# Kernel optimization log

Hardware: AMD Instinct MI355X
Metric: run time of the kernel (lower is better)

## Reference

```python
import jax, jax.numpy as jnp
import numpy as np

B, S, D = 8, 2048, 64
H = 128


def setup_inputs() -> dict:
    key = jax.random.key(0)
    k = jax.random.split(key, 5)
    X = jax.random.normal(k[0], (B, S, D), dtype=jnp.float32)
    Wi = jax.random.normal(k[1], (H, D), dtype=jnp.float32)          # init_layer weight, std=1
    bi = jax.random.normal(k[2], (H,), dtype=jnp.float32)            # init_layer bias, std=1
    Wa = jax.random.normal(k[3], (H * H, D + 1), dtype=jnp.float32) / jnp.sqrt(H)  # vf_A, std=1/sqrt(H)
    Wb = jax.random.normal(k[4], (H, D + 1), dtype=jnp.float32)      # vf_B, std=1
    return {"X": X, "Wi": Wi, "bi": bi, "Wa": Wa, "Wb": Wb}


def reference(X, Wi, bi, Wa, Wb):
    b, s, d = X.shape
    dt = 1.0 / (s - 1)
    # inp: time channel (constant dt) concatenated with scaled input -> [b, s, d+1]
    inp = jnp.concatenate([jnp.full((b, s, 1), dt, dtype=X.dtype), X * dt], axis=-1)
    y0 = X[:, 0] @ Wi.T + bi                       # [b, H]
    Bs = jnp.einsum('bsk,hk->bsh', inp[:, 1:], Wb)  # [b, s-1, H]

    def step(y, xs):
        inp_t, b_t = xs                            # [b, d+1], [b, H]
        A = (inp_t @ Wa.T).reshape(b, H, H)        # per-step transition matrix
        y_new = y + jnp.einsum('bij,bj->bi', A, y) + b_t
        return y_new, y_new

    xs = (jnp.swapaxes(inp[:, 1:], 0, 1), jnp.swapaxes(Bs, 0, 1))  # time-major
    _, ys_rest = jax.lax.scan(step, y0, xs)        # [s-1, b, H]
    ys = jnp.concatenate([y0[:, None, :], jnp.swapaxes(ys_rest, 0, 1)], axis=1)
    return ys
```

## Files before the change

### kernel.cpp

```cpp
#include <hip/hip_runtime.h>
#include <hip/hip_fp16.h>


typedef _Float16 h8 __attribute__((ext_vector_type(8)));
typedef float v4f __attribute__((ext_vector_type(4)));
typedef unsigned int uint;

constexpr int B_ = 8, S_ = 2048, D_ = 64, H_ = 128;
constexpr int T_ = S_ - 1;
constexpr int KD = D_ + 1;
constexpr float DTC = 1.0f / 2047.0f;
constexpr int L_ = 8;
constexpr int LSH = 3;
constexpr int NC = 256;

__global__ __launch_bounds__(256) void k_prep_wa(const float* __restrict__ Wa,
                                                 _Float16* __restrict__ Wa16B,
                                                 float* __restrict__ Wa0) {
  int idx = blockIdx.x * 256 + threadIdx.x;
  int r = idx >> 6, kk = idx & 63;
  int rt = r >> 4, n = r & 15;
  int kb = kk >> 5, q = (kk >> 3) & 3, jj = kk & 7;
  float v = Wa[(size_t)r * KD + 1 + kk];
  Wa16B[((((size_t)rt * 2 + kb) * 4 + q) * 16 + n) * 8 + jj] = (_Float16)v;
  if (kk == 0) Wa0[r] = Wa[(size_t)r * KD];
}

__global__ __launch_bounds__(256) void k_prep_x(const float* __restrict__ X,
                                                _Float16* __restrict__ Xs16) {
  int idx = blockIdx.x * 256 + threadIdx.x;
  int bt = idx >> 6, d = idx & 63;
  int b = bt / T_, s = bt - b * T_;
  Xs16[(size_t)bt * 64 + d] = (_Float16)(X[((size_t)b * S_ + s + 1) * D_ + d] * DTC);
}

__global__ __launch_bounds__(128) void k_y0(const float* __restrict__ X,
                                            const float* __restrict__ Wi,
                                            const float* __restrict__ bi,
                                            float* __restrict__ out,
                                            float* __restrict__ ybound) {
  int b = blockIdx.x, h = threadIdx.x;
  __shared__ float xs[D_];
  if (h < D_) xs[h] = X[(size_t)b * S_ * D_ + h];
  __syncthreads();
  float acc = bi[h];
  const float* wr = Wi + h * D_;
#pragma unroll 8
  for (int d = 0; d < D_; d++) acc += xs[d] * wr[d];
  out[(size_t)b * S_ * H_ + h] = acc;
  if (ybound) ybound[(size_t)(b * NC + 0) * H_ + h] = acc;
}

__global__ __launch_bounds__(256) void k_bs(const float* __restrict__ X,
                                            const float* __restrict__ Wb,
                                            float* __restrict__ Bs) {
  __shared__ float wb_s[H_ * KD];
  __shared__ float xs[16][D_ + 4];
  int tid = threadIdx.x;
  int bt0 = blockIdx.x * 16;
  for (int i = tid; i < H_ * KD; i += 256) wb_s[i] = Wb[i];
  for (int i = tid; i < 16 * D_; i += 256) {
    int sl = i >> 6, d = i & 63;
    int btg = bt0 + sl;
    float v = 0.f;
    if (btg < B_ * T_) {
      int b = btg / T_, s = btg - b * T_;
      v = X[((size_t)b * S_ + s + 1) * D_ + d] * DTC;
    }
    xs[sl][d] = v;
  }
  __syncthreads();
  int h = tid & 127, sh = tid >> 7;
  const float* wrow = &wb_s[h * KD];
  for (int u = 0; u < 8; u++) {
    int sl = sh * 8 + u;
    int btg = bt0 + sl;
    if (btg >= B_ * T_) break;
    float acc = wrow[0] * DTC;
#pragma unroll 8
    for (int d = 0; d < D_; d++) acc += xs[sl][d] * wrow[1 + d];
    Bs[(size_t)btg * H_ + h] = acc;
  }
}

__global__ __launch_bounds__(256) void k_amat(const _Float16* __restrict__ Xs16,
                                              const _Float16* __restrict__ Wa16B,
                                              const float* __restrict__ Wa0,
                                              _Float16* __restrict__ A_sl,
                                              int c0, int scShift) {
  __shared__ _Float16 sb[32 * 528];
  int tid = threadIdx.x;
  int w = tid >> 6, lane = tid & 63;
  int n = lane & 15, q = lane >> 4;
  int rowbase = blockIdx.x * 32;
  int SCm = ((1 << scShift) << LSH) - 1;

  h8 af[2][2];
#pragma unroll
  for (int mi = 0; mi < 2; mi++) {
    int sidx = rowbase + mi * 16 + n;
    int b = sidx >> (scShift + LSH);
    int rem = sidx & SCm;
    int cc = rem >> LSH, l = rem & (L_ - 1);
    int s = (c0 + cc) * L_ + l;
    if (s >= T_) s = T_ - 1;
    size_t btg = (size_t)b * T_ + s;
#pragma unroll
    for (int kb = 0; kb < 2; kb++)
      af[mi][kb] = *(const h8*)(Xs16 + btg * 64 + kb * 32 + q * 8);
  }

  v4f acc[2][8];
#pragma unroll
  for (int nj = 0; nj < 8; nj++) {
    int ct_g = blockIdx.y * 32 + w * 8 + nj;
    float binit = DTC * Wa0[ct_g * 16 + n];
    h8 bf0 = *(const h8*)(Wa16B + ((((size_t)ct_g * 2 + 0) * 4 + q) * 16 + n) * 8);
    h8 bf1 = *(const h8*)(Wa16B + ((((size_t)ct_g * 2 + 1) * 4 + q) * 16 + n) * 8);
#pragma unroll
    for (int mi = 0; mi < 2; mi++) {
      v4f a;
      a[0] = binit; a[1] = binit; a[2] = binit; a[3] = binit;
      a = __builtin_amdgcn_mfma_f32_16x16x32_f16(af[mi][0], bf0, a, 0, 0, 0);
      a = __builtin_amdgcn_mfma_f32_16x16x32_f16(af[mi][1], bf1, a, 0, 0, 0);
      acc[mi][nj] = a;
    }
  }
#pragma unroll
  for (int mi = 0; mi < 2; mi++)
#pragma unroll
    for (int nj = 0; nj < 8; nj++)
#pragma unroll
      for (int reg = 0; reg < 4; reg++)
        sb[(mi * 16 + q * 4 + reg) * 528 + w * 128 + ((nj * 16 + n) ^ (q * 16))] =
            (_Float16)acc[mi][nj][reg];
  __syncthreads();
#pragma unroll
  for (int it = 0; it < 8; it++) {
    int idx = tid + it * 256;
    int t = idx >> 6, u4 = idx & 63;
    int qt = (t >> 2) & 3;
    uint4 val = *(const uint4*)&sb[t * 528 + ((u4 * 8) ^ (qt * 16))];
    *(uint4*)(A_sl + (size_t)(rowbase + t) * 16384 + blockIdx.y * 512 + u4 * 8) = val;
  }
}

__global__ __launch_bounds__(256) void k_chunkmap(const _Float16* __restrict__ A_sl,
                                                  const float* __restrict__ Bs,
                                                  _Float16* __restrict__ Mr,
                                                  float* __restrict__ vch,
                                                  int c0, int scShift) {
  __shared__ _Float16 Dt[128 * 136];
  __shared__ float v32[128];
  int tid = threadIdx.x;
  int w = tid >> 6, lane = tid & 63;
  int n = lane & 15, q = lane >> 4;
  int chunk = blockIdx.x;
  int SC = 1 << scShift;
  int b = chunk >> scShift;
  int cc = chunk & (SC - 1);
  int c = c0 + cc;
  int sbase = c * L_;
  int nsteps = min(L_, T_ - sbase);
  const _Float16* Abase = A_sl + (size_t)chunk * L_ * 16384;
  size_t btb = (size_t)b * T_ + sbase;

#pragma unroll
  for (int it = 0; it < 8; it++) {
    int idx = tid + it * 256;
    int rowl = idx & 127, c8 = (idx >> 7) * 8;
    uint4 pk = *(const uint4*)(Abase + rowl * 128 + c8);
    const _Float16* hp = (const _Float16*)&pk;
#pragma unroll
    for (int cx = 0; cx < 8; cx++) Dt[(c8 + cx) * 136 + rowl] = hp[cx];
  }
  if (tid < 128) v32[tid] = Bs[btb * 128 + tid];
  h8 idE, idO;
#pragma unroll
  for (int jj = 0; jj < 8; jj++) {
    idE[jj] = (_Float16)((q * 8 + jj == n) ? 1.f : 0.f);
    idO[jj] = (_Float16)((q * 8 + jj == 16 + n) ? 1.f : 0.f);
  }
  __syncthreads();

  v4f acc[2][8];
#pragma unroll
  for (int mi = 0; mi < 2; mi++) {
    int row0 = (2 * w + mi) * 16 + q * 4;
#pragma unroll
    for (int nj = 0; nj < 8; nj++) {
      int col = nj * 16 + n;
      union { uint2 u; _Float16 h[4]; } m2;
      m2.u = *(const uint2*)&Dt[col * 136 + row0];
#pragma unroll
      for (int reg = 0; reg < 4; reg++) acc[mi][nj][reg] = (float)m2.h[reg];
    }
  }

  int r0 = 2 * w * 16 + n, r1 = r0 + 16;
  h8 afA[2][4], afB[2][4];

#define LOADA(dst, l)                                                                \
  {                                                                                  \
    const _Float16* Ag = Abase + (size_t)(l) * 16384;                                \
    _Pragma("unroll")                                                                \
    for (int mi = 0; mi < 2; mi++)                                                   \
      _Pragma("unroll")                                                              \
      for (int kb = 0; kb < 4; kb++)                                                 \
        dst[mi][kb] = *(const h8*)(Ag + ((2 * w + mi) * 16 + n) * 128 + kb * 32 + q * 8); \
  }

#define STEPQ(af, l)                                                                 \
  {                                                                                  \
    _Pragma("unroll")                                                                \
    for (int nj = 0; nj < 8; nj++) {                                                 \
      h8 bfr[4];                                                                     \
      _Pragma("unroll")                                                              \
      for (int kb = 0; kb < 4; kb++)                                                 \
        bfr[kb] = *(const h8*)&Dt[(nj * 16 + n) * 136 + kb * 32 + q * 8];            \
      _Pragma("unroll")                                                              \
      for (int mi = 0; mi < 2; mi++) {                                               \
        _Pragma("unroll")                                                            \
        for (int kb = 0; kb < 4; kb++)                                               \
          acc[mi][nj] = __builtin_amdgcn_mfma_f32_16x16x32_f16(af[mi][kb], bfr[kb], acc[mi][nj], 0, 0, 0); \
        acc[mi][nj] = __builtin_amdgcn_mfma_f32_16x16x32_f16(                        \
            af[mi][nj >> 1], (nj & 1) ? idO : idE, acc[mi][nj], 0, 0, 0);            \
      }                                                                              \
    }                                                                                \
    float dv0 = 0.f, dv1 = 0.f;                                                      \
    _Pragma("unroll")                                                                \
    for (int kb = 0; kb < 4; kb++) {                                                 \
      float4 p0 = *(const float4*)&v32[kb * 32 + q * 8];                             \
      float4 p1 = *(const float4*)&v32[kb * 32 + q * 8 + 4];                         \
      float vk[8] = {p0.x, p0.y, p0.z, p0.w, p1.x, p1.y, p1.z, p1.w};                \
      _Pragma("unroll")                                                              \
      for (int jj = 0; jj < 8; jj++) {                                               \
        dv0 += (float)af[0][kb][jj] * vk[jj];                                        \
        dv1 += (float)af[1][kb][jj] * vk[jj];                                        \
      }                                                                              \
    }                                                                                \
    dv0 += __shfl_xor(dv0, 16); dv0 += __shfl_xor(dv0, 32);                          \
    dv1 += __shfl_xor(dv1, 16); dv1 += __shfl_xor(dv1, 32);                          \
    float vold0 = v32[r0], vold1 = v32[r1];                                          \
    float bs0 = 0.f, bs1 = 0.f;                                                      \
    if (q == 0) {                                                                    \
      bs0 = Bs[(btb + (l)) * 128 + r0];                                              \
      bs1 = Bs[(btb + (l)) * 128 + r1];                                              \
    }                                                                                \
    __syncthreads();                                                                 \
    _Pragma("unroll")                                                                \
    for (int mi = 0; mi < 2; mi++) {                                                 \
      int row0 = (2 * w + mi) * 16 + q * 4;                                          \
      _Pragma("unroll")                                                              \
      for (int nj = 0; nj < 8; nj++) {                                               \
        int col = nj * 16 + n;                                                       \
        union { _Float16 h[4]; uint2 u; } pk;                                        \
        _Pragma("unroll")                                                            \
        for (int reg = 0; reg < 4; reg++) pk.h[reg] = (_Float16)acc[mi][nj][reg];    \
        *(uint2*)&Dt[col * 136 + row0] = pk.u;                                       \
      }                                                                              \
    }                                                                                \
    if (q == 0) {                                                                    \
      v32[r0] = vold0 + dv0 + bs0;                                                   \
      v32[r1] = vold1 + dv1 + bs1;                                                   \
    }                                                                                \
    __syncthreads();                                                                 \
  }

  LOADA(afA, 1);
  for (int l = 1; l < nsteps; l += 2) {
    if (l + 1 < nsteps) LOADA(afB, l + 1);
    STEPQ(afA, l);
    if (l + 2 < nsteps) LOADA(afA, l + 2);
    if (l + 1 < nsteps) STEPQ(afB, l + 1);
  }
#undef LOADA
#undef STEPQ

#pragma unroll
  for (int mi = 0; mi < 2; mi++) {
    int row0 = (2 * w + mi) * 16 + q * 4;
#pragma unroll
    for (int nj = 0; nj < 8; nj++) {
      int col = nj * 16 + n;
#pragma unroll
      for (int reg = 0; reg < 4; reg++)
        Dt[(row0 + reg) * 136 + col] = (_Float16)acc[mi][nj][reg];
    }
  }
  __syncthreads();
  _Float16* og = Mr + (size_t)chunk * 16384;
#pragma unroll
  for (int it = 0; it < 8; it++) {
    int idx = tid + it * 256;
    int rowl = idx >> 4, ch = idx & 15;
    uint4 val = *(const uint4*)&Dt[rowl * 136 + ch * 8];
    *(uint4*)(og + rowl * 128 + ch * 8) = val;
  }
  if (tid < 128) vch[(size_t)chunk * 128 + tid] = v32[tid];
}

__global__ __launch_bounds__(256) void k_comp4(const _Float16* __restrict__ in_map,
                                               const float* __restrict__ in_v,
                                               _Float16* __restrict__ out_map,
                                               float* __restrict__ out_v) {
  __shared__ _Float16 Dt[128 * 136];
  __shared__ float v32[128];
  int tid = threadIdx.x;
  int w = tid >> 6, lane = tid & 63;
  int n = lane & 15, q = lane >> 4;
  size_t nbase = (size_t)blockIdx.x * 4;

  const _Float16* P0 = in_map + nbase * 16384;
#pragma unroll
  for (int it = 0; it < 8; it++) {
    int idx = tid + it * 256;
    int rowl = idx & 127, c8 = (idx >> 7) * 8;
    uint4 pk = *(const uint4*)(P0 + rowl * 128 + c8);
    const _Float16* hp = (const _Float16*)&pk;
#pragma unroll
    for (int cx = 0; cx < 8; cx++) Dt[(c8 + cx) * 136 + rowl] = hp[cx];
  }
  if (tid < 128) v32[tid] = in_v[nbase * 128 + tid];
  h8 idE, idO;
#pragma unroll
  for (int jj = 0; jj < 8; jj++) {
    idE[jj] = (_Float16)((q * 8 + jj == n) ? 1.f : 0.f);
    idO[jj] = (_Float16)((q * 8 + jj == 16 + n) ? 1.f : 0.f);
  }
  __syncthreads();

  v4f acc[2][8];
#pragma unroll
  for (int mi = 0; mi < 2; mi++) {
    int row0 = (2 * w + mi) * 16 + q * 4;
#pragma unroll
    for (int nj = 0; nj < 8; nj++) {
      int col = nj * 16 + n;
      union { uint2 u; _Float16 h[4]; } m2;
      m2.u = *(const uint2*)&Dt[col * 136 + row0];
#pragma unroll
      for (int reg = 0; reg < 4; reg++) acc[mi][nj][reg] = (float)m2.h[reg];
    }
  }

  int r0 = 2 * w * 16 + n, r1 = r0 + 16;
  for (int j = 1; j < 4; j++) {
    const _Float16* Pj = in_map + (nbase + j) * 16384;
    h8 af[2][4];
#pragma unroll
    for (int mi = 0; mi < 2; mi++)
#pragma unroll
      for (int kb = 0; kb < 4; kb++)
        af[mi][kb] = *(const h8*)(Pj + ((2 * w + mi) * 16 + n) * 128 + kb * 32 + q * 8);
#pragma unroll
    for (int nj = 0; nj < 8; nj++) {
      h8 bfr[4];
#pragma unroll
      for (int kb = 0; kb < 4; kb++)
        bfr[kb] = *(const h8*)&Dt[(nj * 16 + n) * 136 + kb * 32 + q * 8];
#pragma unroll
      for (int mi = 0; mi < 2; mi++) {
#pragma unroll
        for (int kb = 0; kb < 4; kb++)
          acc[mi][nj] = __builtin_amdgcn_mfma_f32_16x16x32_f16(af[mi][kb], bfr[kb], acc[mi][nj], 0, 0, 0);
        acc[mi][nj] = __builtin_amdgcn_mfma_f32_16x16x32_f16(
            af[mi][nj >> 1], (nj & 1) ? idO : idE, acc[mi][nj], 0, 0, 0);
      }
    }
    float dv0 = 0.f, dv1 = 0.f;
#pragma unroll
    for (int kb = 0; kb < 4; kb++) {
      float4 p0 = *(const float4*)&v32[kb * 32 + q * 8];
      float4 p1 = *(const float4*)&v32[kb * 32 + q * 8 + 4];
      float vk[8] = {p0.x, p0.y, p0.z, p0.w, p1.x, p1.y, p1.z, p1.w};
#pragma unroll
      for (int jj = 0; jj < 8; jj++) {
        dv0 += (float)af[0][kb][jj] * vk[jj];
        dv1 += (float)af[1][kb][jj] * vk[jj];
      }
    }
    dv0 += __shfl_xor(dv0, 16); dv0 += __shfl_xor(dv0, 32);
    dv1 += __shfl_xor(dv1, 16); dv1 += __shfl_xor(dv1, 32);
    float vold0 = v32[r0], vold1 = v32[r1];
    float vj0 = 0.f, vj1 = 0.f;
    if (q == 0) {
      vj0 = in_v[(nbase + j) * 128 + r0];
      vj1 = in_v[(nbase + j) * 128 + r1];
    }
    __syncthreads();
#pragma unroll
    for (int mi = 0; mi < 2; mi++) {
      int row0 = (2 * w + mi) * 16 + q * 4;
#pragma unroll
      for (int nj = 0; nj < 8; nj++) {
        int col = nj * 16 + n;
        union { _Float16 h[4]; uint2 u; } pk;
#pragma unroll
        for (int reg = 0; reg < 4; reg++) pk.h[reg] = (_Float16)acc[mi][nj][reg];
        *(uint2*)&Dt[col * 136 + row0] = pk.u;
      }
    }
    if (q == 0) {
      v32[r0] = vold0 + dv0 + vj0;
      v32[r1] = vold1 + dv1 + vj1;
    }
    __syncthreads();
  }
#pragma unroll
  for (int mi = 0; mi < 2; mi++) {
    int row0 = (2 * w + mi) * 16 + q * 4;
#pragma unroll
    for (int nj = 0; nj < 8; nj++) {
      int col = nj * 16 + n;
#pragma unroll
      for (int reg = 0; reg < 4; reg++)
        Dt[(row0 + reg) * 136 + col] = (_Float16)acc[mi][nj][reg];
    }
  }
  __syncthreads();
  _Float16* og = out_map + (size_t)blockIdx.x * 16384;
#pragma unroll
  for (int it = 0; it < 8; it++) {
    int idx = tid + it * 256;
    int rowl = idx >> 4, ch = idx & 15;
    uint4 val = *(const uint4*)&Dt[rowl * 136 + ch * 8];
    *(uint4*)(og + rowl * 128 + ch * 8) = val;
  }
  if (tid < 128) out_v[(size_t)blockIdx.x * 128 + tid] = v32[tid];
}

__global__ __launch_bounds__(256) void k_chainsuper(const _Float16* __restrict__ Sr,
                                                    const float* __restrict__ sv,
                                                    float* __restrict__ yb,
                                                    int c0, int scShift) {
  int b = blockIdx.x, tid = threadIdx.x;
  int NS = 1 << (scShift - 2);
  int i = tid >> 1, hh = tid & 1;
  __shared__ float ybuf[128];
  __shared__ float red[128];
  if (tid < 128) ybuf[tid] = yb[(size_t)(b * NC + c0) * 128 + tid];
  __syncthreads();

  uint4 arA[8], arB[8];
  float svA, svB;

#define LOADS(ar, svv, s)                                                            \
  {                                                                                  \
    const uint4* p = (const uint4*)(Sr + (size_t)(b * NS + (s)) * 16384 + i * 128 + hh * 64); \
    _Pragma("unroll")                                                                \
    for (int u = 0; u < 8; u++) ar[u] = p[u];                                        \
    svv = sv[(size_t)(b * NS + (s)) * 128 + i];                                      \
  }

#define STEPS(ar, svv, s)                                                            \
  {                                                                                  \
    float pt = 0.f;                                                                  \
    _Pragma("unroll")                                                                \
    for (int u = 0; u < 8; u++) {                                                    \
      union { uint4 v; _Float16 h[8]; } wv; wv.v = ar[u];                            \
      _Pragma("unroll")                                                              \
      for (int k = 0; k < 8; k++) pt += (float)wv.h[k] * ybuf[hh * 64 + u * 8 + k];  \
    }                                                                                \
    if (hh) red[i] = pt;                                                             \
    __syncthreads();                                                                 \
    if (!hh) {                                                                       \
      float yn = ybuf[i] + pt + red[i] + svv;                                        \
      int cg = c0 + 4 * ((s) + 1);                                                   \
      if (cg < NC) yb[(size_t)(b * NC + cg) * 128 + i] = yn;                         \
      ybuf[i] = yn;                                                                  \
    }                                                                                \
    __syncthreads();                                                                 \
  }

  LOADS(arA, svA, 0);
  int s = 0;
  for (; s + 1 < NS; s += 2) {
    LOADS(arB, svB, s + 1);
    STEPS(arA, svA, s);
    if (s + 2 < NS) LOADS(arA, svA, s + 2);
    STEPS(arB, svB, s + 1);
  }
  if (s < NS) STEPS(arA, svA, s);
#undef LOADS
#undef STEPS
}

__global__ __launch_bounds__(256) void k_fill(const _Float16* __restrict__ Mr,
                                              const float* __restrict__ vch,
                                              float* __restrict__ yb,
                                              int c0, int scShift) {
  int tid = threadIdx.x;
  int NS = 1 << (scShift - 2);
  int b = blockIdx.x >> (scShift - 2);
  int s = blockIdx.x & (NS - 1);
  int i = tid >> 1, hh = tid & 1;
  __shared__ float ybuf[128];
  __shared__ float red[128];
  if (tid < 128) ybuf[tid] = yb[(size_t)(b * NC + c0 + 4 * s) * 128 + tid];
  __syncthreads();
  size_t node0 = ((size_t)b << scShift) + 4 * s;

  uint4 arA[8], arB[8];
  float vvA, vvB;

#define LOADF(ar, vv, k)                                                             \
  {                                                                                  \
    const uint4* p = (const uint4*)(Mr + (node0 + (k)) * 16384 + i * 128 + hh * 64); \
    _Pragma("unroll")                                                                \
    for (int u = 0; u < 8; u++) ar[u] = p[u];                                        \
    vv = vch[(node0 + (k)) * 128 + i];                                               \
  }

#define STEPF(ar, vv, k)                                                             \
  {                                                                                  \
    float pt = 0.f;                                                                  \
    _Pragma("unroll")                                                                \
    for (int u = 0; u < 8; u++) {                                                    \
      union { uint4 v; _Float16 h[8]; } wv; wv.v = ar[u];                            \
      _Pragma("unroll")                                                              \
      for (int kk = 0; kk < 8; kk++) pt += (float)wv.h[kk] * ybuf[hh * 64 + u * 8 + kk]; \
    }                                                                                \
    if (hh) red[i] = pt;                                                             \
    __syncthreads();                                                                 \
    if (!hh) {                                                                       \
      float yn = ybuf[i] + pt + red[i] + vv;                                         \
      yb[(size_t)(b * NC + c0 + 4 * s + (k) + 1) * 128 + i] = yn;                    \
      ybuf[i] = yn;                                                                  \
    }                                                                                \
    __syncthreads();                                                                 \
  }

  LOADF(arA, vvA, 0);
  LOADF(arB, vvB, 1);
  STEPF(arA, vvA, 0);
  LOADF(arA, vvA, 2);
  STEPF(arB, vvB, 1);
  STEPF(arA, vvA, 2);
#undef LOADF
#undef STEPF
}

__global__ __launch_bounds__(256) void k_emit(const _Float16* __restrict__ A_sl,
                                              const float* __restrict__ Bs,
                                              const float* __restrict__ yb,
                                              float* __restrict__ out,
                                              int c0, int scShift) {
  int tid = threadIdx.x;
  int SC = 1 << scShift;
  int b = blockIdx.x >> scShift;
  int cc = blockIdx.x & (SC - 1);
  int c = c0 + cc;
  int i = tid >> 1, hh = tid & 1;
  __shared__ float ybuf[128];
  __shared__ float red[128];
  if (tid < 128) ybuf[tid] = yb[(size_t)(b * NC + c) * 128 + tid];
  __syncthreads();
  int nst = min(L_, T_ - c * L_);
  size_t sidx0 = (size_t)blockIdx.x * L_;
  size_t btb = (size_t)b * T_ + c * L_;

  uint4 arA[8], arB[8];
  float bsA, bsB;

#define LOADR(ar, bsv, l)                                                            \
  {                                                                                  \
    const uint4* p = (const uint4*)(A_sl + (sidx0 + (l)) * 16384 + i * 128 + hh * 64); \
    _Pragma("unroll")                                                                \
    for (int u = 0; u < 8; u++) ar[u] = p[u];                                        \
    bsv = Bs[(btb + (l)) * 128 + i];                                                 \
  }

#define STEPE(ar, bsv, l)                                                            \
  {                                                                                  \
    float pt = 0.f;                                                                  \
    _Pragma("unroll")                                                                \
    for (int u = 0; u < 8; u++) {                                                    \
      union { uint4 v; _Float16 h[8]; } wv; wv.v = ar[u];                            \
      _Pragma("unroll")                                                              \
      for (int k = 0; k < 8; k++) pt += (float)wv.h[k] * ybuf[hh * 64 + u * 8 + k];  \
    }                                                                                \
    if (hh) red[i] = pt;                                                             \
    __syncthreads();                                                                 \
    if (!hh) {                                                                       \
      float yn = ybuf[i] + pt + red[i] + bsv;                                        \
      out[((size_t)b * S_ + (size_t)(c * L_ + (l) + 1)) * 128 + i] = yn;             \
      ybuf[i] = yn;                                                                  \
    }                                                                                \
    __syncthreads();                                                                 \
  }

  LOADR(arA, bsA, 0);
  for (int l = 0; l < nst; l += 2) {
    if (l + 1 < nst) LOADR(arB, bsB, l + 1);
    STEPE(arA, bsA, l);
    if (l + 2 < nst) LOADR(arA, bsA, l + 2);
    if (l + 1 < nst) STEPE(arB, bsB, l + 1);
  }
#undef LOADR
#undef STEPE
}

__global__ __launch_bounds__(256) void k_seq(const float* __restrict__ X,
                                             const float* __restrict__ Wa,
                                             const float* __restrict__ Wb,
                                             float* __restrict__ out) {
  int b = blockIdx.x, tid = threadIdx.x;
  int i = tid >> 1, hh = tid & 1;
  __shared__ float y[H_], red[H_], xs[D_], bts[H_];
  if (tid < H_) y[tid] = out[(size_t)b * S_ * H_ + tid];
  __syncthreads();
  for (int t = 1; t < S_; t++) {
    if (tid < D_) xs[tid] = X[((size_t)b * S_ + t) * D_ + tid] * DTC;
    __syncthreads();
    if (tid < H_) {
      const float* wr = Wb + tid * KD;
      float acc = wr[0] * DTC;
#pragma unroll 8
      for (int d = 0; d < D_; d++) acc += xs[d] * wr[1 + d];
      bts[tid] = acc;
    }
    float part = 0.f;
    const float* yhalf = &y[hh * 64];
    for (int j = 0; j < 64; j++) {
      const float* wr = Wa + ((size_t)(i * H_) + hh * 64 + j) * KD;
      float a = wr[0] * DTC;
#pragma unroll 8
      for (int d = 0; d < D_; d++) a += xs[d] * wr[1 + d];
      part += a * yhalf[j];
    }
    if (hh) red[i] = part;
    __syncthreads();
    if (!hh) {
      float yn = y[i] + part + red[i] + bts[i];
      out[((size_t)b * S_ + t) * H_ + i] = yn;
      y[i] = yn;
    }
    __syncthreads();
  }
}

extern "C" void kernel_launch(void* const* d_in, const int* in_sizes, int n_in,
                              void* d_out, int out_size, void* d_ws, size_t ws_size,
                              hipStream_t stream) {
  (void)in_sizes; (void)n_in; (void)out_size;
  const float* X  = (const float*)d_in[0];
  const float* Wi = (const float*)d_in[1];
  const float* bi = (const float*)d_in[2];
  const float* Wa = (const float*)d_in[3];
  const float* Wb = (const float*)d_in[4];
  float* out = (float*)d_out;
  char* ws = (char*)d_ws;

  size_t off = 0;
  auto alloc = [&](size_t bytes) { size_t o = off; off = (off + bytes + 255) & ~(size_t)255; return o; };
  size_t oBs  = alloc((size_t)B_ * T_ * 128 * 4);
  size_t oYb  = alloc((size_t)B_ * NC * 128 * 4);
  size_t oWaB = alloc((size_t)64 * 16384 * 2);
  size_t oWa0 = alloc((size_t)16384 * 4);
  size_t oXs  = alloc((size_t)B_ * T_ * 64 * 2);
  size_t fixed = off;

  const size_t APC  = (size_t)B_ * L_ * 16384 * 2;
  const size_t MRPC = (size_t)B_ * 16384 * 2;
  const size_t VCPC = (size_t)B_ * 128 * 4;
  const size_t SRPC = (size_t)B_ * 16384 * 2 / 4;
  const size_t SVPC = (size_t)B_ * 128;
  const size_t PER_SC = APC + MRPC + VCPC + SRPC + SVPC + 5 * 256;

  int SC = 0;
  if (ws_size > fixed) {
    size_t avail = ws_size - fixed;
    SC = 64;
    while (SC >= 4 && (size_t)SC * PER_SC > avail) SC >>= 1;
    if (SC < 4) SC = 0;
  }
  if (SC < 4) {
    k_y0<<<B_, 128, 0, stream>>>(X, Wi, bi, out, nullptr);
    k_seq<<<B_, 256, 0, stream>>>(X, Wa, Wb, out);
    return;
  }
  int scShift = __builtin_ctz(SC);

  size_t oMr = alloc((size_t)SC * MRPC);
  size_t oVc = alloc((size_t)SC * VCPC);
  size_t oSr = alloc((size_t)SC * SRPC);
  size_t oSv = alloc((size_t)SC * SVPC);
  size_t oA  = alloc((size_t)SC * APC);

  float*    Bs    = (float*)(ws + oBs);
  float*    yb    = (float*)(ws + oYb);
  _Float16* Wa16B = (_Float16*)(ws + oWaB);
  float*    Wa0   = (float*)(ws + oWa0);
  _Float16* Xs16  = (_Float16*)(ws + oXs);
  _Float16* Mr    = (_Float16*)(ws + oMr);
  float*    vch   = (float*)(ws + oVc);
  _Float16* Sr    = (_Float16*)(ws + oSr);
  float*    sv    = (float*)(ws + oSv);
  _Float16* A_sl  = (_Float16*)(ws + oA);

  k_prep_wa<<<4096, 256, 0, stream>>>(Wa, Wa16B, Wa0);
  k_prep_x<<<4094, 256, 0, stream>>>(X, Xs16);
  k_y0<<<B_, 128, 0, stream>>>(X, Wi, bi, out, yb);
  k_bs<<<(B_ * T_ + 15) / 16, 256, 0, stream>>>(X, Wb, Bs);

  int nslices = NC / SC;
  int chunks = B_ * SC;
  int amat_gx = (B_ * SC * L_) / 32;
  for (int si = 0; si < nslices; si++) {
    int c0 = si * SC;
    k_amat<<<dim3(amat_gx, 32), 256, 0, stream>>>(Xs16, Wa16B, Wa0, A_sl, c0, scShift);
    k_chunkmap<<<chunks, 256, 0, stream>>>(A_sl, Bs, Mr, vch, c0, scShift);
    k_comp4<<<chunks / 4, 256, 0, stream>>>(Mr, vch, Sr, sv);
    k_chainsuper<<<B_, 256, 0, stream>>>(Sr, sv, yb, c0, scShift);
    k_fill<<<chunks / 4, 256, 0, stream>>>(Mr, vch, yb, c0, scShift);
    k_emit<<<chunks, 256, 0, stream>>>(A_sl, Bs, yb, out, c0, scShift);
  }
}
```

Before: 616.1 us.

## Fuse prep kernels and fold chunk-boundary fill into emit kernel

Merges the Wa/X conversion kernels into one launch and the y0/Bs kernels into another, which cuts launch count. Removes the separate k_fill pass: each emit block now recomputes its own chunk starting state by applying up to three chunk maps from the super-chunk boundary in shared memory. This saves one launch per slice and the global round trip for boundary states. In exchange, emit blocks do redundant serial mat-vec work and read extra Mr data, and the work is uneven across blocks.

```diff
diff --git a/kernel.cpp b/kernel.cpp
--- a/kernel.cpp
+++ b/kernel.cpp
@@ -14,49 +14,55 @@
 constexpr int LSH = 3;
 constexpr int NC = 256;
 
-__global__ __launch_bounds__(256) void k_prep_wa(const float* __restrict__ Wa,
-                                                 _Float16* __restrict__ Wa16B,
-                                                 float* __restrict__ Wa0) {
-  int idx = blockIdx.x * 256 + threadIdx.x;
-  int r = idx >> 6, kk = idx & 63;
-  int rt = r >> 4, n = r & 15;
-  int kb = kk >> 5, q = (kk >> 3) & 3, jj = kk & 7;
-  float v = Wa[(size_t)r * KD + 1 + kk];
-  Wa16B[((((size_t)rt * 2 + kb) * 4 + q) * 16 + n) * 8 + jj] = (_Float16)v;
-  if (kk == 0) Wa0[r] = Wa[(size_t)r * KD];
-}
-
-__global__ __launch_bounds__(256) void k_prep_x(const float* __restrict__ X,
-                                                _Float16* __restrict__ Xs16) {
-  int idx = blockIdx.x * 256 + threadIdx.x;
-  int bt = idx >> 6, d = idx & 63;
-  int b = bt / T_, s = bt - b * T_;
-  Xs16[(size_t)bt * 64 + d] = (_Float16)(X[((size_t)b * S_ + s + 1) * D_ + d] * DTC);
-}
-
-__global__ __launch_bounds__(128) void k_y0(const float* __restrict__ X,
-                                            const float* __restrict__ Wi,
-                                            const float* __restrict__ bi,
-                                            float* __restrict__ out,
-                                            float* __restrict__ ybound) {
-  int b = blockIdx.x, h = threadIdx.x;
-  __shared__ float xs[D_];
-  if (h < D_) xs[h] = X[(size_t)b * S_ * D_ + h];
-  __syncthreads();
-  float acc = bi[h];
-  const float* wr = Wi + h * D_;
+__global__ __launch_bounds__(256) void k_prep0(const float* __restrict__ Wa,
+                                               _Float16* __restrict__ Wa16B,
+                                               float* __restrict__ Wa0,
+                                               const float* __restrict__ X,
+                                               _Float16* __restrict__ Xs16) {
+  int bx = blockIdx.x;
+  if (bx < 4096) {
+    int idx = bx * 256 + threadIdx.x;
+    int r = idx >> 6, kk = idx & 63;
+    int rt = r >> 4, n = r & 15;
+    int kb = kk >> 5, q = (kk >> 3) & 3, jj = kk & 7;
+    float v = Wa[(size_t)r * KD + 1 + kk];
+    Wa16B[((((size_t)rt * 2 + kb) * 4 + q) * 16 + n) * 8 + jj] = (_Float16)v;
+    if (kk == 0) Wa0[r] = Wa[(size_t)r * KD];
+  } else {
+    int idx = (bx - 4096) * 256 + threadIdx.x;
+    if (idx < B_ * T_ * 64) {
+      int bt = idx >> 6, d = idx & 63;
+      int b = bt / T_, s = bt - b * T_;
+      Xs16[(size_t)bt * 64 + d] = (_Float16)(X[((size_t)b * S_ + s + 1) * D_ + d] * DTC);
+    }
+  }
+}
+
+__global__ __launch_bounds__(256) void k_prep1(const float* __restrict__ X,
+                                               const float* __restrict__ Wb,
+                                               float* __restrict__ Bs,
+                                               const float* __restrict__ Wi,
+                                               const float* __restrict__ bi,
+                                               float* __restrict__ out,
+                                               float* __restrict__ yb) {
+  int tid = threadIdx.x;
+  if (blockIdx.x >= 1024) {
+    int b = blockIdx.x - 1024;
+    __shared__ float xs0[D_];
+    if (tid < D_) xs0[tid] = X[(size_t)b * S_ * D_ + tid];
+    __syncthreads();
+    if (tid < H_) {
+      float acc = bi[tid];
+      const float* wr = Wi + tid * D_;
 #pragma unroll 8
-  for (int d = 0; d < D_; d++) acc += xs[d] * wr[d];
-  out[(size_t)b * S_ * H_ + h] = acc;
-  if (ybound) ybound[(size_t)(b * NC + 0) * H_ + h] = acc;
-}
-
-__global__ __launch_bounds__(256) void k_bs(const float* __restrict__ X,
-                                            const float* __restrict__ Wb,
-                                            float* __restrict__ Bs) {
+      for (int d = 0; d < D_; d++) acc += xs0[d] * wr[d];
+      out[(size_t)b * S_ * H_ + tid] = acc;
+      yb[(size_t)(b * NC + 0) * H_ + tid] = acc;
+    }
+    return;
+  }
   __shared__ float wb_s[H_ * KD];
   __shared__ float xs[16][D_ + 4];
-  int tid = threadIdx.x;
   int bt0 = blockIdx.x * 16;
   for (int i = tid; i < H_ * KD; i += 256) wb_s[i] = Wb[i];
   for (int i = tid; i < 16 * D_; i += 256) {
@@ -486,63 +492,10 @@
 #undef STEPS
 }
 
-__global__ __launch_bounds__(256) void k_fill(const _Float16* __restrict__ Mr,
-                                              const float* __restrict__ vch,
-                                              float* __restrict__ yb,
-                                              int c0, int scShift) {
-  int tid = threadIdx.x;
-  int NS = 1 << (scShift - 2);
-  int b = blockIdx.x >> (scShift - 2);
-  int s = blockIdx.x & (NS - 1);
-  int i = tid >> 1, hh = tid & 1;
-  __shared__ float ybuf[128];
-  __shared__ float red[128];
-  if (tid < 128) ybuf[tid] = yb[(size_t)(b * NC + c0 + 4 * s) * 128 + tid];
-  __syncthreads();
-  size_t node0 = ((size_t)b << scShift) + 4 * s;
-
-  uint4 arA[8], arB[8];
-  float vvA, vvB;
-
-#define LOADF(ar, vv, k)                                                             \
-  {                                                                                  \
-    const uint4* p = (const uint4*)(Mr + (node0 + (k)) * 16384 + i * 128 + hh * 64); \
-    _Pragma("unroll")                                                                \
-    for (int u = 0; u < 8; u++) ar[u] = p[u];                                        \
-    vv = vch[(node0 + (k)) * 128 + i];                                               \
-  }
-
-#define STEPF(ar, vv, k)                                                             \
-  {                                                                                  \
-    float pt = 0.f;                                                                  \
-    _Pragma("unroll")                                                                \
-    for (int u = 0; u < 8; u++) {                                                    \
-      union { uint4 v; _Float16 h[8]; } wv; wv.v = ar[u];                            \
-      _Pragma("unroll")                                                              \
-      for (int kk = 0; kk < 8; kk++) pt += (float)wv.h[kk] * ybuf[hh * 64 + u * 8 + kk]; \
-    }                                                                                \
-    if (hh) red[i] = pt;                                                             \
-    __syncthreads();                                                                 \
-    if (!hh) {                                                                       \
-      float yn = ybuf[i] + pt + red[i] + vv;                                         \
-      yb[(size_t)(b * NC + c0 + 4 * s + (k) + 1) * 128 + i] = yn;                    \
-      ybuf[i] = yn;                                                                  \
-    }                                                                                \
-    __syncthreads();                                                                 \
-  }
-
-  LOADF(arA, vvA, 0);
-  LOADF(arB, vvB, 1);
-  STEPF(arA, vvA, 0);
-  LOADF(arA, vvA, 2);
-  STEPF(arB, vvB, 1);
-  STEPF(arA, vvA, 2);
-#undef LOADF
-#undef STEPF
-}
-
 __global__ __launch_bounds__(256) void k_emit(const _Float16* __restrict__ A_sl,
                                               const float* __restrict__ Bs,
+                                              const _Float16* __restrict__ Mr,
+                                              const float* __restrict__ vch,
                                               const float* __restrict__ yb,
                                               float* __restrict__ out,
                                               int c0, int scShift) {
@@ -554,14 +507,39 @@
   int i = tid >> 1, hh = tid & 1;
   __shared__ float ybuf[128];
   __shared__ float red[128];
-  if (tid < 128) ybuf[tid] = yb[(size_t)(b * NC + c) * 128 + tid];
-  __syncthreads();
+  int kpre = cc & 3;
+  int cbase = c - kpre;
+  if (tid < 128) ybuf[tid] = yb[(size_t)(b * NC + cbase) * 128 + tid];
+  __syncthreads();
+  size_t node0 = ((size_t)b << scShift) + (cc & ~3);
+
+  uint4 arA[8], arB[8];
+  float bsA, bsB;
+
+  for (int j = 0; j < kpre; j++) {
+    const uint4* p = (const uint4*)(Mr + (node0 + j) * 16384 + i * 128 + hh * 64);
+#pragma unroll
+    for (int u = 0; u < 8; u++) arA[u] = p[u];
+    float vv = vch[(node0 + j) * 128 + i];
+    float pt = 0.f;
+#pragma unroll
+    for (int u = 0; u < 8; u++) {
+      union { uint4 v; _Float16 h[8]; } wv; wv.v = arA[u];
+#pragma unroll
+      for (int k = 0; k < 8; k++) pt += (float)wv.h[k] * ybuf[hh * 64 + u * 8 + k];
+    }
+    if (hh) red[i] = pt;
+    __syncthreads();
+    if (!hh) {
+      float yn = ybuf[i] + pt + red[i] + vv;
+      ybuf[i] = yn;
+    }
+    __syncthreads();
+  }
+
   int nst = min(L_, T_ - c * L_);
   size_t sidx0 = (size_t)blockIdx.x * L_;
   size_t btb = (size_t)b * T_ + c * L_;
-
-  uint4 arA[8], arB[8];
-  float bsA, bsB;
 
 #define LOADR(ar, bsv, l)                                                            \
   {                                                                                  \
@@ -638,6 +616,21 @@
     }
     __syncthreads();
   }
+}
+
+__global__ __launch_bounds__(128) void k_y0f(const float* __restrict__ X,
+                                             const float* __restrict__ Wi,
+                                             const float* __restrict__ bi,
+                                             float* __restrict__ out) {
+  int b = blockIdx.x, h = threadIdx.x;
+  __shared__ float xs[D_];
+  if (h < D_) xs[h] = X[(size_t)b * S_ * D_ + h];
+  __syncthreads();
+  float acc = bi[h];
+  const float* wr = Wi + h * D_;
+#pragma unroll 8
+  for (int d = 0; d < D_; d++) acc += xs[d] * wr[d];
+  out[(size_t)b * S_ * H_ + h] = acc;
 }
 
 extern "C" void kernel_launch(void* const* d_in, const int* in_sizes, int n_in,
@@ -676,7 +669,7 @@
     if (SC < 4) SC = 0;
   }
   if (SC < 4) {
-    k_y0<<<B_, 128, 0, stream>>>(X, Wi, bi, out, nullptr);
+    k_y0f<<<B_, 128, 0, stream>>>(X, Wi, bi, out);
     k_seq<<<B_, 256, 0, stream>>>(X, Wa, Wb, out);
     return;
   }
@@ -699,10 +692,8 @@
   float*    sv    = (float*)(ws + oSv);
   _Float16* A_sl  = (_Float16*)(ws + oA);
 
-  k_prep_wa<<<4096, 256, 0, stream>>>(Wa, Wa16B, Wa0);
-  k_prep_x<<<4094, 256, 0, stream>>>(X, Xs16);
-  k_y0<<<B_, 128, 0, stream>>>(X, Wi, bi, out, yb);
-  k_bs<<<(B_ * T_ + 15) / 16, 256, 0, stream>>>(X, Wb, Bs);
+  k_prep0<<<4096 + 4094, 256, 0, stream>>>(Wa, Wa16B, Wa0, X, Xs16);
+  k_prep1<<<1024 + B_, 256, 0, stream>>>(X, Wb, Bs, Wi, bi, out, yb);
 
   int nslices = NC / SC;
   int chunks = B_ * SC;
@@ -713,7 +704,6 @@
     k_chunkmap<<<chunks, 256, 0, stream>>>(A_sl, Bs, Mr, vch, c0, scShift);
     k_comp4<<<chunks / 4, 256, 0, stream>>>(Mr, vch, Sr, sv);
     k_chainsuper<<<B_, 256, 0, stream>>>(Sr, sv, yb, c0, scShift);
-    k_fill<<<chunks / 4, 256, 0, stream>>>(Mr, vch, yb, c0, scShift);
-    k_emit<<<chunks, 256, 0, stream>>>(A_sl, Bs, yb, out, c0, scShift);
-  }
-}
+    k_emit<<<chunks, 256, 0, stream>>>(A_sl, Bs, Mr, vch, yb, out, c0, scShift);
+  }
+}
```

New measurement: 608.3 us. Within noise of the previous version (-1.3%).
